# Optimization experiments

Measured on AMD Instinct MI355X. Metric: run time of the kernel, lower is better.

The kernel has to match this reference:

```python
import jax, jax.numpy as jnp
import numpy as np

B, N, H = 8, 256, 768
P = 128          # path_hidden_size
HEADS = 12
D = H // HEADS   # 64
EPS = 1e-5


def layer_norm(x, g, b):
    mu = jnp.mean(x, axis=-1, keepdims=True)
    var = jnp.mean((x - mu) ** 2, axis=-1, keepdims=True)
    return (x - mu) * jax.lax.rsqrt(var + EPS) * g + b


def setup_inputs() -> dict:
    key = jax.random.key(0)
    ks = jax.random.split(key, 16)
    s = 0.02
    return {
        "nodes": jax.random.normal(ks[0], (B, N, H), jnp.float32),
        "bias": jax.random.normal(ks[1], (B, HEADS, N, N), jnp.float32),
        "paths": jax.random.normal(ks[2], (B, N, N, P), jnp.float32),
        "Wq": jax.random.normal(ks[3], (H, H), jnp.float32) * s,
        "bq": jnp.zeros((H,), jnp.float32),
        "Wk": jax.random.normal(ks[4], (H, H), jnp.float32) * s,
        "bk": jnp.zeros((H,), jnp.float32),
        "Wv": jax.random.normal(ks[5], (H, H), jnp.float32) * s,
        "bv": jnp.zeros((H,), jnp.float32),
        "Wsk": jax.random.normal(ks[6], (P, D), jnp.float32) * s,
        "bsk": jnp.zeros((D,), jnp.float32),
        "Wsv": jax.random.normal(ks[7], (P, D), jnp.float32) * s,
        "bsv": jnp.zeros((D,), jnp.float32),
        "Wo": jax.random.normal(ks[8], (H, H), jnp.float32) * s,
        "bo": jnp.zeros((H,), jnp.float32),
        "g_path": jnp.ones((P,), jnp.float32),
        "b_path": jnp.zeros((P,), jnp.float32),
        "g_out": jnp.ones((H,), jnp.float32),
        "b_out": jnp.zeros((H,), jnp.float32),
    }


def reference(nodes, bias, paths, Wq, bq, Wk, bk, Wv, bv, Wsk, bsk, Wsv, bsv,
              Wo, bo, g_path, b_path, g_out, b_out):
    # q/k/v: [B,N,H] -> [B,heads,N,D]
    def split(x):
        return x.reshape(B, N, HEADS, D).transpose(0, 2, 1, 3)

    q = split(nodes @ Wq + bq)
    k = split(nodes @ Wk + bk)
    v = split(nodes @ Wv + bv)

    pn = layer_norm(paths, g_path, b_path)          # [B,N,N,P]
    struct_k = pn @ Wsk + bsk                       # [B,N,N,D]
    struct_v = pn @ Wsv + bsv                       # [B,N,N,D]

    q = q * (D ** -0.5)
    # content scores + per-query-row structural scores + bias
    w = (jnp.einsum('bhqd,bhkd->bhqk', q, k)
         + jnp.einsum('bhqd,bqkd->bhqk', q, struct_k)
         + bias)
    w = jax.nn.softmax(w, axis=-1)                  # [B,heads,N,N]

    out = (jnp.einsum('bhqk,bhkd->bhqd', w, v)
           + jnp.einsum('bhqk,bqkd->bhqd', w, struct_v))
    out = out.transpose(0, 2, 1, 3).reshape(B, N, H)  # combine heads
    out = jax.nn.relu(out @ Wo + bo)
    # dropout is identity in eval mode
    return layer_norm(nodes + out, g_out, b_out)
```

## Files before the change

### kernel.cpp

```cpp
#include <hip/hip_runtime.h>
#include <stdint.h>

#define Bb 8
#define Nn 256
#define Hh 768
#define Pp 128
#define HEADS 12
#define Dd 64
#define EPSf 1e-5f

typedef __attribute__((ext_vector_type(8))) short bhalf8;
typedef __attribute__((ext_vector_type(4))) float f32x4;

__device__ __forceinline__ unsigned short f2bf(float f) {
    union { float f; unsigned u; } v; v.f = f;
    unsigned r = v.u + 0x7FFFu + ((v.u >> 16) & 1u);
    return (unsigned short)(r >> 16);
}

__global__ __launch_bounds__(256) void k_transpose4(const float* __restrict__ a0, const float* __restrict__ a1,
                                                    const float* __restrict__ a2, const float* __restrict__ a3,
                                                    unsigned short* __restrict__ o0, unsigned short* __restrict__ o1,
                                                    unsigned short* __restrict__ o2, unsigned short* __restrict__ o3) {
    __shared__ float tile[32][33];
    int z = blockIdx.z;
    const float* in = (z == 0) ? a0 : (z == 1) ? a1 : (z == 2) ? a2 : a3;
    unsigned short* out = (z == 0) ? o0 : (z == 1) ? o1 : (z == 2) ? o2 : o3;
    const int R = 768, C = 768;
    int c0 = blockIdx.x * 32, r0 = blockIdx.y * 32;
    int tx = threadIdx.x & 31, ty = threadIdx.x >> 5;
    for (int i = ty; i < 32; i += 8)
        tile[i][tx] = in[(size_t)(r0 + i) * C + c0 + tx];
    __syncthreads();
    for (int i = ty; i < 32; i += 8)
        out[(size_t)(c0 + i) * R + r0 + tx] = f2bf(tile[tx][i]);
}

__global__ __launch_bounds__(256) void k_transpose_small(const float* __restrict__ a0, const float* __restrict__ a1,
                                                         unsigned short* __restrict__ o0, unsigned short* __restrict__ o1) {
    __shared__ float tile[32][33];
    int z = blockIdx.z;
    const float* in = (z == 0) ? a0 : a1;
    unsigned short* out = (z == 0) ? o0 : o1;
    const int R = 128, C = 64;
    int c0 = blockIdx.x * 32, r0 = blockIdx.y * 32;
    int tx = threadIdx.x & 31, ty = threadIdx.x >> 5;
    for (int i = ty; i < 32; i += 8)
        tile[i][tx] = in[(size_t)(r0 + i) * C + c0 + tx];
    __syncthreads();
    for (int i = ty; i < 32; i += 8)
        out[(size_t)(c0 + i) * R + r0 + tx] = f2bf(tile[tx][i]);
}

__global__ __launch_bounds__(256) void k_qkv(const float* __restrict__ nodes,
                                             const unsigned short* __restrict__ Wt,
                                             const float* __restrict__ bq, const float* __restrict__ bk,
                                             const float* __restrict__ bv,
                                             float* __restrict__ qs, float* __restrict__ kk,
                                             float* __restrict__ vv) {
    __shared__ __align__(16) unsigned short Alds[64 * 72];
    __shared__ __align__(16) unsigned short Blds[128 * 72];
    int tid = threadIdx.x;
    int m0 = blockIdx.y * 64;
    int n0 = blockIdx.x * 128;
    int w = tid >> 6, lane = tid & 63;
    int wm = w >> 1, wn = w & 1;
    int lm = lane & 15, lq = lane >> 4;
    f32x4 acc[2][4];
#pragma unroll
    for (int i = 0; i < 2; i++)
#pragma unroll
        for (int j = 0; j < 4; j++) acc[i][j] = (f32x4){0.f, 0.f, 0.f, 0.f};

    for (int kt = 0; kt < 768; kt += 64) {
#pragma unroll
        for (int t = 0; t < 4; t++) {
            int c = t * 256 + tid;
            int row = c >> 4, cc = c & 15;
            float4 v = *(const float4*)(nodes + (size_t)(m0 + row) * 768 + kt + cc * 4);
            uint2 uu;
            uu.x = (unsigned)f2bf(v.x) | ((unsigned)f2bf(v.y) << 16);
            uu.y = (unsigned)f2bf(v.z) | ((unsigned)f2bf(v.w) << 16);
            *(uint2*)(Alds + row * 72 + cc * 4) = uu;
        }
#pragma unroll
        for (int t = 0; t < 4; t++) {
            int c = t * 256 + tid;
            int n = c >> 3, kc = c & 7;
            uint4 v = *(const uint4*)(Wt + (size_t)(n0 + n) * 768 + kt + kc * 8);
            *(uint4*)(Blds + n * 72 + kc * 8) = v;
        }
        __syncthreads();
#pragma unroll
        for (int ks = 0; ks < 2; ks++) {
            bhalf8 af[2];
#pragma unroll
            for (int mi = 0; mi < 2; mi++)
                af[mi] = *(const bhalf8*)(Alds + (wm * 32 + mi * 16 + lm) * 72 + ks * 32 + lq * 8);
#pragma unroll
            for (int nt = 0; nt < 4; nt++) {
                bhalf8 bf = *(const bhalf8*)(Blds + (wn * 64 + nt * 16 + lm) * 72 + ks * 32 + lq * 8);
#pragma unroll
                for (int mi = 0; mi < 2; mi++)
                    acc[mi][nt] = __builtin_amdgcn_mfma_f32_16x16x32_bf16(af[mi], bf, acc[mi][nt], 0, 0, 0);
            }
        }
        __syncthreads();
    }
    int wsel = n0 / 768;
    int nb = n0 % 768;
    const float* bias = (wsel == 0) ? bq : (wsel == 1) ? bk : bv;
    float* dst = (wsel == 0) ? qs : (wsel == 1) ? kk : vv;
    float scale = (wsel == 0) ? 0.125f : 1.0f;
#pragma unroll
    for (int mi = 0; mi < 2; mi++)
#pragma unroll
        for (int nt = 0; nt < 4; nt++)
#pragma unroll
            for (int r = 0; r < 4; r++) {
                int row = m0 + wm * 32 + mi * 16 + lq * 4 + r;
                int col = nb + wn * 64 + nt * 16 + lm;
                int hh = col >> 6, d = col & 63;
                int b = row >> 8, qn = row & 255;
                float val = (acc[mi][nt][r] + bias[col]) * scale;
                dst[(((size_t)b * HEADS + hh) * Nn + qn) * Dd + d] = val;
            }
}

__global__ __launch_bounds__(256) void k_scores(const float* __restrict__ qs,
                                                const float* __restrict__ kk,
                                                const float* __restrict__ bias,
                                                float* __restrict__ wg) {
    __shared__ __align__(16) unsigned short Alds[64 * 72];
    __shared__ __align__(16) unsigned short Blds[64 * 72];
    int tid = threadIdx.x;
    int bh = blockIdx.z;
    int m0 = blockIdx.y * 64;
    int n0 = blockIdx.x * 64;
    int w = tid >> 6, lane = tid & 63, lm = lane & 15, lq = lane >> 4;
    const float* Abase = qs + ((size_t)bh * Nn + m0) * Dd;
    const float* Bbase = kk + ((size_t)bh * Nn + n0) * Dd;
#pragma unroll
    for (int t = 0; t < 4; t++) {
        int c = t * 256 + tid;
        int row = c >> 4, cc = c & 15;
        float4 va = *(const float4*)(Abase + (size_t)row * 64 + cc * 4);
        uint2 ua;
        ua.x = (unsigned)f2bf(va.x) | ((unsigned)f2bf(va.y) << 16);
        ua.y = (unsigned)f2bf(va.z) | ((unsigned)f2bf(va.w) << 16);
        *(uint2*)(Alds + row * 72 + cc * 4) = ua;
        float4 vb = *(const float4*)(Bbase + (size_t)row * 64 + cc * 4);
        uint2 ub;
        ub.x = (unsigned)f2bf(vb.x) | ((unsigned)f2bf(vb.y) << 16);
        ub.y = (unsigned)f2bf(vb.z) | ((unsigned)f2bf(vb.w) << 16);
        *(uint2*)(Blds + row * 72 + cc * 4) = ub;
    }
    __syncthreads();
    f32x4 acc[4];
#pragma unroll
    for (int i = 0; i < 4; i++) acc[i] = (f32x4){0.f, 0.f, 0.f, 0.f};
#pragma unroll
    for (int ks = 0; ks < 2; ks++) {
        bhalf8 af = *(const bhalf8*)(Alds + (w * 16 + lm) * 72 + ks * 32 + lq * 8);
#pragma unroll
        for (int nt = 0; nt < 4; nt++) {
            bhalf8 bf = *(const bhalf8*)(Blds + (nt * 16 + lm) * 72 + ks * 32 + lq * 8);
            acc[nt] = __builtin_amdgcn_mfma_f32_16x16x32_bf16(af, bf, acc[nt], 0, 0, 0);
        }
    }
#pragma unroll
    for (int nt = 0; nt < 4; nt++)
#pragma unroll
        for (int r = 0; r < 4; r++) {
            int row = m0 + w * 16 + lq * 4 + r;
            int col = n0 + nt * 16 + lm;
            size_t idx = ((size_t)bh * Nn + row) * Nn + col;
            wg[idx] = acc[nt][r] + bias[idx];
        }
}

__global__ __launch_bounds__(256) void k_structproj(const float* __restrict__ paths,
                                                    const unsigned short* __restrict__ Wskvt,
                                                    const float* __restrict__ gp, const float* __restrict__ bp,
                                                    const float* __restrict__ bsk, const float* __restrict__ bsv,
                                                    unsigned short* __restrict__ skv) {
    __shared__ __align__(16) unsigned short pn[64 * 136];
    __shared__ __align__(16) unsigned short Bt[128 * 136];
    int tid = threadIdx.x;
    size_t r0 = (size_t)blockIdx.x * 64;
    int w = tid >> 6, lane = tid & 63, lm = lane & 15, lq = lane >> 4;
#pragma unroll
    for (int t = 0; t < 8; t++) {
        int c = t * 256 + tid;
        int n = c >> 4, kc = c & 15;
        uint4 v = *(const uint4*)(Wskvt + n * 128 + kc * 8);
        *(uint4*)(Bt + n * 136 + kc * 8) = v;
    }
    float4 g0 = *(const float4*)(gp + lm * 4);
    float4 g1 = *(const float4*)(gp + 64 + lm * 4);
    float4 bb0 = *(const float4*)(bp + lm * 4);
    float4 bb1 = *(const float4*)(bp + 64 + lm * 4);
#pragma unroll
    for (int it = 0; it < 4; it++) {
        int row_l = w * 16 + it * 4 + lq;
        size_t row = r0 + row_l;
        const float* pr = paths + row * 128;
        float4 x0 = *(const float4*)(pr + lm * 4);
        float4 x1 = *(const float4*)(pr + 64 + lm * 4);
        float s = (x0.x + x0.y) + (x0.z + x0.w) + (x1.x + x1.y) + (x1.z + x1.w);
        float s2 = x0.x * x0.x + x0.y * x0.y + x0.z * x0.z + x0.w * x0.w
                 + x1.x * x1.x + x1.y * x1.y + x1.z * x1.z + x1.w * x1.w;
#pragma unroll
        for (int mk = 1; mk < 16; mk <<= 1) {
            s += __shfl_xor(s, mk);
            s2 += __shfl_xor(s2, mk);
        }
        float mu = s * (1.f / 128.f);
        float var = s2 * (1.f / 128.f) - mu * mu;
        float rs = rsqrtf(var + EPSf);
        float p0 = (x0.x - mu) * rs * g0.x + bb0.x;
        float p1 = (x0.y - mu) * rs * g0.y + bb0.y;
        float p2 = (x0.z - mu) * rs * g0.z + bb0.z;
        float p3 = (x0.w - mu) * rs * g0.w + bb0.w;
        float p4 = (x1.x - mu) * rs * g1.x + bb1.x;
        float p5 = (x1.y - mu) * rs * g1.y + bb1.y;
        float p6 = (x1.z - mu) * rs * g1.z + bb1.z;
        float p7 = (x1.w - mu) * rs * g1.w + bb1.w;
        uint2 ua, ub;
        ua.x = (unsigned)f2bf(p0) | ((unsigned)f2bf(p1) << 16);
        ua.y = (unsigned)f2bf(p2) | ((unsigned)f2bf(p3) << 16);
        ub.x = (unsigned)f2bf(p4) | ((unsigned)f2bf(p5) << 16);
        ub.y = (unsigned)f2bf(p6) | ((unsigned)f2bf(p7) << 16);
        *(uint2*)(pn + row_l * 136 + lm * 4) = ua;
        *(uint2*)(pn + row_l * 136 + 64 + lm * 4) = ub;
    }
    __syncthreads();
    f32x4 acc[8];
#pragma unroll
    for (int i = 0; i < 8; i++) acc[i] = (f32x4){0.f, 0.f, 0.f, 0.f};
#pragma unroll
    for (int ks = 0; ks < 4; ks++) {
        bhalf8 af = *(const bhalf8*)(pn + (w * 16 + lm) * 136 + ks * 32 + lq * 8);
#pragma unroll
        for (int nt = 0; nt < 8; nt++) {
            bhalf8 bf = *(const bhalf8*)(Bt + (nt * 16 + lm) * 136 + ks * 32 + lq * 8);
            acc[nt] = __builtin_amdgcn_mfma_f32_16x16x32_bf16(af, bf, acc[nt], 0, 0, 0);
        }
    }
    __syncthreads();
#pragma unroll
    for (int nt = 0; nt < 8; nt++) {
        int col = nt * 16 + lm;
        float bias = (col < 64) ? bsk[col] : bsv[col - 64];
#pragma unroll
        for (int r = 0; r < 4; r++) {
            int row_l = w * 16 + lq * 4 + r;
            pn[row_l * 136 + col] = f2bf(acc[nt][r] + bias);
        }
    }
    __syncthreads();
#pragma unroll
    for (int i = 0; i < 4; i++) {
        int c = i * 256 + tid;
        int row = c >> 4, chunk = c & 15;
        uint4 v = *(const uint4*)(pn + row * 136 + chunk * 8);
        *(uint4*)(skv + (r0 + row) * 128 + chunk * 8) = v;
    }
}

__global__ __launch_bounds__(256) void k_attn(const float* __restrict__ qs,
                                              const unsigned short* __restrict__ skv,
                                              float* __restrict__ wg,
                                              float* __restrict__ attn) {
    __shared__ __align__(16) unsigned short SKV[256 * 72];
    __shared__ __align__(16) unsigned short A2[16 * 264];
    __shared__ __align__(16) unsigned short Ql[16 * 72];
    __shared__ float redm[16][4];
    __shared__ float reds[16][4];
    int tid = threadIdx.x;
    int bq = blockIdx.x;
    int b = bq >> 8, q = bq & 255;
    int w = tid >> 6, lane = tid & 63, lm = lane & 15, lq = lane >> 4;
    if (tid < 192) {
        int h = tid >> 4, dc = (tid & 15) * 4;
        float4 v = *(const float4*)(qs + (((size_t)b * HEADS + h) * Nn + q) * Dd + dc);
        uint2 u;
        u.x = (unsigned)f2bf(v.x) | ((unsigned)f2bf(v.y) << 16);
        u.y = (unsigned)f2bf(v.z) | ((unsigned)f2bf(v.w) << 16);
        *(uint2*)(Ql + h * 72 + dc) = u;
    } else {
        int t = tid - 192;
        int h = 12 + (t >> 4), dc = (t & 15) * 4;
        uint2 z; z.x = 0; z.y = 0;
        *(uint2*)(Ql + h * 72 + dc) = z;
    }
    const unsigned short* rowb = skv + (size_t)bq * 256 * 128;
#pragma unroll
    for (int i = 0; i < 8; i++) {
        int c = i * 256 + tid;
        int k = c >> 3, j = c & 7;
        uint4 v = *(const uint4*)(rowb + (size_t)k * 128 + j * 8);
        *(uint4*)(SKV + k * 72 + j * 8) = v;
    }
    __syncthreads();
    f32x4 acc1[4];
#pragma unroll
    for (int i = 0; i < 4; i++) acc1[i] = (f32x4){0.f, 0.f, 0.f, 0.f};
#pragma unroll
    for (int ks = 0; ks < 2; ks++) {
        bhalf8 af = *(const bhalf8*)(Ql + lm * 72 + ks * 32 + lq * 8);
#pragma unroll
        for (int nt = 0; nt < 4; nt++) {
            int n0 = (w * 4 + nt) * 16;
            bhalf8 bf = *(const bhalf8*)(SKV + (n0 + lm) * 72 + ks * 32 + lq * 8);
            acc1[nt] = __builtin_amdgcn_mfma_f32_16x16x32_bf16(af, bf, acc1[nt], 0, 0, 0);
        }
    }
    size_t wbase = ((size_t)b * HEADS) * Nn * Nn + (size_t)q * Nn;
    float S[4][4];
#pragma unroll
    for (int nt = 0; nt < 4; nt++)
#pragma unroll
        for (int r = 0; r < 4; r++) {
            int row = lq * 4 + r;
            int col = (w * 4 + nt) * 16 + lm;
            float wgv = (row < 12) ? wg[wbase + (size_t)row * (Nn * Nn) + col] : 0.f;
            S[nt][r] = acc1[nt][r] + wgv;
        }
    float m4[4];
#pragma unroll
    for (int r = 0; r < 4; r++)
        m4[r] = fmaxf(fmaxf(S[0][r], S[1][r]), fmaxf(S[2][r], S[3][r]));
#pragma unroll
    for (int mk = 1; mk < 16; mk <<= 1)
#pragma unroll
        for (int r = 0; r < 4; r++) m4[r] = fmaxf(m4[r], __shfl_xor(m4[r], mk));
    if (lm == 0) {
#pragma unroll
        for (int r = 0; r < 4; r++) redm[lq * 4 + r][w] = m4[r];
    }
    __syncthreads();
    float rowmax[4];
#pragma unroll
    for (int r = 0; r < 4; r++) {
        int row = lq * 4 + r;
        rowmax[r] = fmaxf(fmaxf(redm[row][0], redm[row][1]), fmaxf(redm[row][2], redm[row][3]));
    }
    float P[4][4], psum[4];
#pragma unroll
    for (int r = 0; r < 4; r++) {
#pragma unroll
        for (int nt = 0; nt < 4; nt++) P[nt][r] = __expf(S[nt][r] - rowmax[r]);
        psum[r] = (P[0][r] + P[1][r]) + (P[2][r] + P[3][r]);
    }
#pragma unroll
    for (int mk = 1; mk < 16; mk <<= 1)
#pragma unroll
        for (int r = 0; r < 4; r++) psum[r] += __shfl_xor(psum[r], mk);
    if (lm == 0) {
#pragma unroll
        for (int r = 0; r < 4; r++) reds[lq * 4 + r][w] = psum[r];
    }
    __syncthreads();
    float inv[4];
#pragma unroll
    for (int r = 0; r < 4; r++) {
        int row = lq * 4 + r;
        inv[r] = 1.f / (((reds[row][0] + reds[row][1]) + (reds[row][2] + reds[row][3])));
    }
#pragma unroll
    for (int nt = 0; nt < 4; nt++)
#pragma unroll
        for (int r = 0; r < 4; r++) {
            int row = lq * 4 + r;
            int col = (w * 4 + nt) * 16 + lm;
            float p = P[nt][r] * inv[r];
            A2[row * 264 + col] = f2bf(p);
            if (row < 12) wg[wbase + (size_t)row * (Nn * Nn) + col] = p;
        }
#pragma unroll
    for (int i = 0; i < 8; i++) {
        int c = i * 256 + tid;
        int k = c >> 3, j = c & 7;
        uint4 v = *(const uint4*)(rowb + (size_t)k * 128 + 64 + j * 8);
        *(uint4*)(SKV + k * 72 + j * 8) = v;
    }
    __syncthreads();
    f32x4 acc2 = (f32x4){0.f, 0.f, 0.f, 0.f};
#pragma unroll
    for (int ks = 0; ks < 8; ks++) {
        bhalf8 af = *(const bhalf8*)(A2 + lm * 264 + ks * 32 + lq * 8);
        bhalf8 bf;
#pragma unroll
        for (int j = 0; j < 8; j++)
            bf[j] = (short)SKV[(ks * 32 + lq * 8 + j) * 72 + w * 16 + lm];
        acc2 = __builtin_amdgcn_mfma_f32_16x16x32_bf16(af, bf, acc2, 0, 0, 0);
    }
#pragma unroll
    for (int r = 0; r < 4; r++) {
        int row = lq * 4 + r;
        if (row < 12) attn[(size_t)bq * Hh + row * 64 + w * 16 + lm] = acc2[r];
    }
}

__global__ __launch_bounds__(256) void k_ctxout(const float* __restrict__ wg,
                                                const float* __restrict__ vv,
                                                float* __restrict__ attn) {
    __shared__ __align__(16) float Al[64 * 68];
    __shared__ __align__(16) float Bl[64 * 68];
    int tid = threadIdx.x;
    int bh = blockIdx.y;
    int m0 = blockIdx.x * 64;
    int b = bh / 12, h = bh % 12;
    int tx = tid & 15, ty = tid >> 4;
    int c0 = tx * 4, r0 = ty * 4;
    float acc[4][4];
#pragma unroll
    for (int i = 0; i < 4; i++)
#pragma unroll
        for (int j = 0; j < 4; j++) acc[i][j] = 0.f;
    const float* Abase = wg + ((size_t)bh * Nn + m0) * Nn;
    const float* Bbase = vv + (size_t)bh * Nn * Dd;
    for (int kt = 0; kt < 256; kt += 64) {
#pragma unroll
        for (int t = 0; t < 4; t++) {
            int c = t * 256 + tid;
            int row = c >> 4, cc = c & 15;
            *(float4*)(Al + row * 68 + cc * 4) = *(const float4*)(Abase + (size_t)row * 256 + kt + cc * 4);
            *(float4*)(Bl + row * 68 + cc * 4) = *(const float4*)(Bbase + (size_t)(kt + row) * 64 + cc * 4);
        }
        __syncthreads();
#pragma unroll 8
        for (int k = 0; k < 64; k++) {
            float4 bv4 = *(const float4*)(Bl + k * 68 + c0);
            float a0 = Al[(r0 + 0) * 68 + k];
            float a1 = Al[(r0 + 1) * 68 + k];
            float a2 = Al[(r0 + 2) * 68 + k];
            float a3 = Al[(r0 + 3) * 68 + k];
            acc[0][0] += a0 * bv4.x; acc[0][1] += a0 * bv4.y; acc[0][2] += a0 * bv4.z; acc[0][3] += a0 * bv4.w;
            acc[1][0] += a1 * bv4.x; acc[1][1] += a1 * bv4.y; acc[1][2] += a1 * bv4.z; acc[1][3] += a1 * bv4.w;
            acc[2][0] += a2 * bv4.x; acc[2][1] += a2 * bv4.y; acc[2][2] += a2 * bv4.z; acc[2][3] += a2 * bv4.w;
            acc[3][0] += a3 * bv4.x; acc[3][1] += a3 * bv4.y; acc[3][2] += a3 * bv4.z; acc[3][3] += a3 * bv4.w;
        }
        __syncthreads();
    }
#pragma unroll
    for (int i = 0; i < 4; i++)
#pragma unroll
        for (int j = 0; j < 4; j++) {
            size_t o = ((size_t)b * Nn + m0 + r0 + i) * Hh + h * 64 + c0 + j;
            attn[o] += acc[i][j];
        }
}

__global__ __launch_bounds__(256) void k_outproj(const float* __restrict__ attn,
                                                 const unsigned short* __restrict__ Wot,
                                                 const float* __restrict__ bo,
                                                 const float* __restrict__ nodes,
                                                 float* __restrict__ tmp) {
    __shared__ __align__(16) unsigned short Alds[64 * 72];
    __shared__ __align__(16) unsigned short Blds[128 * 72];
    int tid = threadIdx.x;
    int m0 = blockIdx.y * 64;
    int n0 = blockIdx.x * 128;
    int w = tid >> 6, lane = tid & 63;
    int wm = w >> 1, wn = w & 1;
    int lm = lane & 15, lq = lane >> 4;
    f32x4 acc[2][4];
#pragma unroll
    for (int i = 0; i < 2; i++)
#pragma unroll
        for (int j = 0; j < 4; j++) acc[i][j] = (f32x4){0.f, 0.f, 0.f, 0.f};
    for (int kt = 0; kt < 768; kt += 64) {
#pragma unroll
        for (int t = 0; t < 4; t++) {
            int c = t * 256 + tid;
            int row = c >> 4, cc = c & 15;
            float4 v = *(const float4*)(attn + (size_t)(m0 + row) * 768 + kt + cc * 4);
            uint2 uu;
            uu.x = (unsigned)f2bf(v.x) | ((unsigned)f2bf(v.y) << 16);
            uu.y = (unsigned)f2bf(v.z) | ((unsigned)f2bf(v.w) << 16);
            *(uint2*)(Alds + row * 72 + cc * 4) = uu;
        }
#pragma unroll
        for (int t = 0; t < 4; t++) {
            int c = t * 256 + tid;
            int n = c >> 3, kc = c & 7;
            uint4 v = *(const uint4*)(Wot + (size_t)(n0 + n) * 768 + kt + kc * 8);
            *(uint4*)(Blds + n * 72 + kc * 8) = v;
        }
        __syncthreads();
#pragma unroll
        for (int ks = 0; ks < 2; ks++) {
            bhalf8 af[2];
#pragma unroll
            for (int mi = 0; mi < 2; mi++)
                af[mi] = *(const bhalf8*)(Alds + (wm * 32 + mi * 16 + lm) * 72 + ks * 32 + lq * 8);
#pragma unroll
            for (int nt = 0; nt < 4; nt++) {
                bhalf8 bf = *(const bhalf8*)(Blds + (wn * 64 + nt * 16 + lm) * 72 + ks * 32 + lq * 8);
#pragma unroll
                for (int mi = 0; mi < 2; mi++)
                    acc[mi][nt] = __builtin_amdgcn_mfma_f32_16x16x32_bf16(af[mi], bf, acc[mi][nt], 0, 0, 0);
            }
        }
        __syncthreads();
    }
#pragma unroll
    for (int mi = 0; mi < 2; mi++)
#pragma unroll
        for (int nt = 0; nt < 4; nt++)
#pragma unroll
            for (int r = 0; r < 4; r++) {
                int row = m0 + wm * 32 + mi * 16 + lq * 4 + r;
                int col = n0 + wn * 64 + nt * 16 + lm;
                float val = acc[mi][nt][r] + bo[col];
                val = fmaxf(val, 0.f) + nodes[(size_t)row * 768 + col];
                tmp[(size_t)row * 768 + col] = val;
            }
}

__global__ __launch_bounds__(256) void k_finalln(const float* __restrict__ tmp,
                                                 const float* __restrict__ go,
                                                 const float* __restrict__ bout,
                                                 float* __restrict__ out) {
    __shared__ float rs1[4], rs2[4];
    int m = blockIdx.x, tid = threadIdx.x;
    int lane = tid & 63, wid = tid >> 6;
    const float* row = tmp + (size_t)m * 768;
    float x0 = row[tid], x1 = row[tid + 256], x2 = row[tid + 512];
    float s = x0 + x1 + x2;
    float s2 = x0 * x0 + x1 * x1 + x2 * x2;
#pragma unroll
    for (int mk = 32; mk; mk >>= 1) {
        s += __shfl_xor(s, mk);
        s2 += __shfl_xor(s2, mk);
    }
    if (lane == 0) { rs1[wid] = s; rs2[wid] = s2; }
    __syncthreads();
    s = rs1[0] + rs1[1] + rs1[2] + rs1[3];
    s2 = rs2[0] + rs2[1] + rs2[2] + rs2[3];
    float mu = s * (1.f / 768.f);
    float var = s2 * (1.f / 768.f) - mu * mu;
    float rstd = rsqrtf(var + EPSf);
    float* orow = out + (size_t)m * 768;
    orow[tid] = (x0 - mu) * rstd * go[tid] + bout[tid];
    orow[tid + 256] = (x1 - mu) * rstd * go[tid + 256] + bout[tid + 256];
    orow[tid + 512] = (x2 - mu) * rstd * go[tid + 512] + bout[tid + 512];
}

extern "C" void kernel_launch(void* const* d_in, const int* in_sizes, int n_in,
                              void* d_out, int out_size, void* d_ws, size_t ws_size,
                              hipStream_t stream) {
    const float* nodes = (const float*)d_in[0];
    const float* bias  = (const float*)d_in[1];
    const float* paths = (const float*)d_in[2];
    const float* Wq = (const float*)d_in[3];  const float* bq  = (const float*)d_in[4];
    const float* Wk = (const float*)d_in[5];  const float* bk  = (const float*)d_in[6];
    const float* Wv = (const float*)d_in[7];  const float* bv  = (const float*)d_in[8];
    const float* Wsk = (const float*)d_in[9]; const float* bsk = (const float*)d_in[10];
    const float* Wsv = (const float*)d_in[11];const float* bsv = (const float*)d_in[12];
    const float* Wo = (const float*)d_in[13]; const float* bo  = (const float*)d_in[14];
    const float* gp = (const float*)d_in[15]; const float* bp  = (const float*)d_in[16];
    const float* go = (const float*)d_in[17]; const float* bout= (const float*)d_in[18];
    float* out = (float*)d_out;

    char* ws = (char*)d_ws;
    size_t off = 0;
    auto carve = [&](size_t bytes) -> char* {
        char* p = ws + off;
        off += (bytes + 255) & ~(size_t)255;
        return p;
    };
    float* qs   = (float*)carve((size_t)Bb * HEADS * Nn * Dd * 4);
    float* kk   = (float*)carve((size_t)Bb * HEADS * Nn * Dd * 4);
    float* vv   = (float*)carve((size_t)Bb * HEADS * Nn * Dd * 4);
    float* wg   = (float*)carve((size_t)Bb * HEADS * Nn * Nn * 4);
    float* attn = (float*)carve((size_t)Bb * Nn * Hh * 4);
    float* tmp  = (float*)carve((size_t)Bb * Nn * Hh * 4);
    unsigned short* Wqkvt = (unsigned short*)carve((size_t)3 * 768 * 768 * 2);
    unsigned short* Wot   = (unsigned short*)carve((size_t)768 * 768 * 2);
    unsigned short* Wskvt = (unsigned short*)carve((size_t)128 * 128 * 2);
    unsigned short* skv   = (unsigned short*)carve((size_t)Bb * Nn * Nn * 128 * 2);
    (void)ws_size; (void)in_sizes; (void)n_in; (void)out_size;

    hipLaunchKernelGGL(k_transpose4, dim3(24, 24, 4), dim3(256), 0, stream,
                       Wq, Wk, Wv, Wo,
                       Wqkvt, Wqkvt + (size_t)768 * 768, Wqkvt + (size_t)2 * 768 * 768, Wot);
    hipLaunchKernelGGL(k_transpose_small, dim3(2, 4, 2), dim3(256), 0, stream,
                       Wsk, Wsv, Wskvt, Wskvt + (size_t)64 * 128);

    hipLaunchKernelGGL(k_qkv, dim3(18, 32), dim3(256), 0, stream, nodes, Wqkvt, bq, bk, bv, qs, kk, vv);
    hipLaunchKernelGGL(k_scores, dim3(4, 4, 96), dim3(256), 0, stream, qs, kk, bias, wg);
    hipLaunchKernelGGL(k_structproj, dim3(8192), dim3(256), 0, stream, paths, Wskvt, gp, bp, bsk, bsv, skv);
    hipLaunchKernelGGL(k_attn, dim3(2048), dim3(256), 0, stream, qs, skv, wg, attn);
    hipLaunchKernelGGL(k_ctxout, dim3(4, 96), dim3(256), 0, stream, wg, vv, attn);
    hipLaunchKernelGGL(k_outproj, dim3(6, 32), dim3(256), 0, stream, attn, Wot, bo, nodes, tmp);
    hipLaunchKernelGGL(k_finalln, dim3(2048), dim3(256), 0, stream, tmp, go, bout, out);
}
```

Before: 557.4 us.

## Restructure attention pipeline with bf16 transposed layouts and MFMA context GEMM

The pipeline now keeps intermediates in bf16 in transposed layouts: V is stored as [B,H,D,N], the struct projection writes separate struct-K and transposed struct-V buffers, and the softmax probabilities are written as bf16. The context GEMM moves from scalar FP32 FMA to bf16 MFMA. The QKV and output GEMMs read B fragments straight from global memory and double-buffer the A tile in LDS. A cheaper bf16 pack using perm replaces the round-to-nearest-even conversion, which trades exact rounding for fewer instructions. The struct projection processes 128 rows per block, halving the grid, and reads weights from global memory instead of LDS.

```diff
diff --git a/kernel.cpp b/kernel.cpp
--- a/kernel.cpp
+++ b/kernel.cpp
@@ -16,6 +16,11 @@
     union { float f; unsigned u; } v; v.f = f;
     unsigned r = v.u + 0x7FFFu + ((v.u >> 16) & 1u);
     return (unsigned short)(r >> 16);
+}
+__device__ __forceinline__ unsigned pk(float lo, float hi) {
+    unsigned a = __float_as_uint(lo) + 0x8000u;
+    unsigned b = __float_as_uint(hi) + 0x8000u;
+    return __builtin_amdgcn_perm(b, a, 0x07060302u);
 }
 
 __global__ __launch_bounds__(256) void k_transpose4(const float* __restrict__ a0, const float* __restrict__ a1,
@@ -54,52 +59,48 @@
 
 __global__ __launch_bounds__(256) void k_qkv(const float* __restrict__ nodes,
                                              const unsigned short* __restrict__ Wt,
-                                             const float* __restrict__ bq, const float* __restrict__ bk,
-                                             const float* __restrict__ bv,
-                                             float* __restrict__ qs, float* __restrict__ kk,
-                                             float* __restrict__ vv) {
-    __shared__ __align__(16) unsigned short Alds[64 * 72];
-    __shared__ __align__(16) unsigned short Blds[128 * 72];
+                                             const float* __restrict__ bqp, const float* __restrict__ bkp,
+                                             const float* __restrict__ bvp,
+                                             float* __restrict__ qso, float* __restrict__ kko,
+                                             unsigned short* __restrict__ vvT) {
+    __shared__ __align__(16) unsigned short A[2][64 * 72];
     int tid = threadIdx.x;
     int m0 = blockIdx.y * 64;
     int n0 = blockIdx.x * 128;
     int w = tid >> 6, lane = tid & 63;
     int wm = w >> 1, wn = w & 1;
     int lm = lane & 15, lq = lane >> 4;
-    f32x4 acc[2][4];
-#pragma unroll
-    for (int i = 0; i < 2; i++)
-#pragma unroll
-        for (int j = 0; j < 4; j++) acc[i][j] = (f32x4){0.f, 0.f, 0.f, 0.f};
-
-    for (int kt = 0; kt < 768; kt += 64) {
+
+    auto stageA = [&](int kt, unsigned short* dst) {
 #pragma unroll
         for (int t = 0; t < 4; t++) {
             int c = t * 256 + tid;
             int row = c >> 4, cc = c & 15;
             float4 v = *(const float4*)(nodes + (size_t)(m0 + row) * 768 + kt + cc * 4);
-            uint2 uu;
-            uu.x = (unsigned)f2bf(v.x) | ((unsigned)f2bf(v.y) << 16);
-            uu.y = (unsigned)f2bf(v.z) | ((unsigned)f2bf(v.w) << 16);
-            *(uint2*)(Alds + row * 72 + cc * 4) = uu;
-        }
-#pragma unroll
-        for (int t = 0; t < 4; t++) {
-            int c = t * 256 + tid;
-            int n = c >> 3, kc = c & 7;
-            uint4 v = *(const uint4*)(Wt + (size_t)(n0 + n) * 768 + kt + kc * 8);
-            *(uint4*)(Blds + n * 72 + kc * 8) = v;
-        }
-        __syncthreads();
+            uint2 u; u.x = pk(v.x, v.y); u.y = pk(v.z, v.w);
+            *(uint2*)(dst + row * 72 + cc * 4) = u;
+        }
+    };
+    f32x4 acc[2][4];
+#pragma unroll
+    for (int i = 0; i < 2; i++)
+#pragma unroll
+        for (int j = 0; j < 4; j++) acc[i][j] = (f32x4){0.f, 0.f, 0.f, 0.f};
+
+    stageA(0, A[0]);
+    __syncthreads();
+    int buf = 0;
+    for (int kt = 0; kt < 768; kt += 64, buf ^= 1) {
+        if (kt < 704) stageA(kt + 64, A[buf ^ 1]);
 #pragma unroll
         for (int ks = 0; ks < 2; ks++) {
             bhalf8 af[2];
 #pragma unroll
             for (int mi = 0; mi < 2; mi++)
-                af[mi] = *(const bhalf8*)(Alds + (wm * 32 + mi * 16 + lm) * 72 + ks * 32 + lq * 8);
+                af[mi] = *(const bhalf8*)(A[buf] + (wm * 32 + mi * 16 + lm) * 72 + ks * 32 + lq * 8);
 #pragma unroll
             for (int nt = 0; nt < 4; nt++) {
-                bhalf8 bf = *(const bhalf8*)(Blds + (wn * 64 + nt * 16 + lm) * 72 + ks * 32 + lq * 8);
+                bhalf8 bf = *(const bhalf8*)(Wt + (size_t)(n0 + wn * 64 + nt * 16 + lm) * 768 + kt + ks * 32 + lq * 8);
 #pragma unroll
                 for (int mi = 0; mi < 2; mi++)
                     acc[mi][nt] = __builtin_amdgcn_mfma_f32_16x16x32_bf16(af[mi], bf, acc[mi][nt], 0, 0, 0);
@@ -109,22 +110,39 @@
     }
     int wsel = n0 / 768;
     int nb = n0 % 768;
-    const float* bias = (wsel == 0) ? bq : (wsel == 1) ? bk : bv;
-    float* dst = (wsel == 0) ? qs : (wsel == 1) ? kk : vv;
-    float scale = (wsel == 0) ? 0.125f : 1.0f;
-#pragma unroll
-    for (int mi = 0; mi < 2; mi++)
-#pragma unroll
-        for (int nt = 0; nt < 4; nt++)
-#pragma unroll
-            for (int r = 0; r < 4; r++) {
-                int row = m0 + wm * 32 + mi * 16 + lq * 4 + r;
+    if (wsel == 2) {
+#pragma unroll
+        for (int mi = 0; mi < 2; mi++)
+#pragma unroll
+            for (int nt = 0; nt < 4; nt++) {
                 int col = nb + wn * 64 + nt * 16 + lm;
-                int hh = col >> 6, d = col & 63;
-                int b = row >> 8, qn = row & 255;
-                float val = (acc[mi][nt][r] + bias[col]) * scale;
-                dst[(((size_t)b * HEADS + hh) * Nn + qn) * Dd + d] = val;
+                int h = col >> 6, d = col & 63;
+                int row0 = m0 + wm * 32 + mi * 16 + lq * 4;
+                int bb = row0 >> 8, q0 = row0 & 255;
+                float bia = bvp[col];
+                uint2 u;
+                u.x = pk(acc[mi][nt][0] + bia, acc[mi][nt][1] + bia);
+                u.y = pk(acc[mi][nt][2] + bia, acc[mi][nt][3] + bia);
+                *(uint2*)(vvT + (((size_t)bb * HEADS + h) * Dd + d) * Nn + q0) = u;
             }
+    } else {
+        const float* bias = (wsel == 0) ? bqp : bkp;
+        float* dst = (wsel == 0) ? qso : kko;
+        float scale = (wsel == 0) ? 0.125f : 1.0f;
+#pragma unroll
+        for (int mi = 0; mi < 2; mi++)
+#pragma unroll
+            for (int nt = 0; nt < 4; nt++)
+#pragma unroll
+                for (int r = 0; r < 4; r++) {
+                    int row = m0 + wm * 32 + mi * 16 + lq * 4 + r;
+                    int col = nb + wn * 64 + nt * 16 + lm;
+                    int hh = col >> 6, d = col & 63;
+                    int bb = row >> 8, qn = row & 255;
+                    float val = (acc[mi][nt][r] + bias[col]) * scale;
+                    dst[(((size_t)bb * HEADS + hh) * Nn + qn) * Dd + d] = val;
+                }
+    }
 }
 
 __global__ __launch_bounds__(256) void k_scores(const float* __restrict__ qs,
@@ -145,14 +163,10 @@
         int c = t * 256 + tid;
         int row = c >> 4, cc = c & 15;
         float4 va = *(const float4*)(Abase + (size_t)row * 64 + cc * 4);
-        uint2 ua;
-        ua.x = (unsigned)f2bf(va.x) | ((unsigned)f2bf(va.y) << 16);
-        ua.y = (unsigned)f2bf(va.z) | ((unsigned)f2bf(va.w) << 16);
+        uint2 ua; ua.x = pk(va.x, va.y); ua.y = pk(va.z, va.w);
         *(uint2*)(Alds + row * 72 + cc * 4) = ua;
         float4 vb = *(const float4*)(Bbase + (size_t)row * 64 + cc * 4);
-        uint2 ub;
-        ub.x = (unsigned)f2bf(vb.x) | ((unsigned)f2bf(vb.y) << 16);
-        ub.y = (unsigned)f2bf(vb.z) | ((unsigned)f2bf(vb.w) << 16);
+        uint2 ub; ub.x = pk(vb.x, vb.y); ub.y = pk(vb.z, vb.w);
         *(uint2*)(Blds + row * 72 + cc * 4) = ub;
     }
     __syncthreads();
@@ -183,28 +197,24 @@
                                                     const unsigned short* __restrict__ Wskvt,
                                                     const float* __restrict__ gp, const float* __restrict__ bp,
                                                     const float* __restrict__ bsk, const float* __restrict__ bsv,
-                                                    unsigned short* __restrict__ skv) {
-    __shared__ __align__(16) unsigned short pn[64 * 136];
-    __shared__ __align__(16) unsigned short Bt[128 * 136];
+                                                    unsigned short* __restrict__ skg,
+                                                    unsigned short* __restrict__ svTg) {
+    __shared__ __align__(16) unsigned short SM[17920];
+    unsigned short* pn  = SM;
+    unsigned short* skl = SM;
+    unsigned short* svl = SM + 9216;
     int tid = threadIdx.x;
-    size_t r0 = (size_t)blockIdx.x * 64;
+    size_t r0 = (size_t)blockIdx.x * 128;
+    int bq = (int)(r0 >> 8), k0 = (int)(r0 & 255);
     int w = tid >> 6, lane = tid & 63, lm = lane & 15, lq = lane >> 4;
-#pragma unroll
-    for (int t = 0; t < 8; t++) {
-        int c = t * 256 + tid;
-        int n = c >> 4, kc = c & 15;
-        uint4 v = *(const uint4*)(Wskvt + n * 128 + kc * 8);
-        *(uint4*)(Bt + n * 136 + kc * 8) = v;
-    }
     float4 g0 = *(const float4*)(gp + lm * 4);
     float4 g1 = *(const float4*)(gp + 64 + lm * 4);
-    float4 bb0 = *(const float4*)(bp + lm * 4);
-    float4 bb1 = *(const float4*)(bp + 64 + lm * 4);
-#pragma unroll
-    for (int it = 0; it < 4; it++) {
-        int row_l = w * 16 + it * 4 + lq;
-        size_t row = r0 + row_l;
-        const float* pr = paths + row * 128;
+    float4 b0 = *(const float4*)(bp + lm * 4);
+    float4 b1 = *(const float4*)(bp + 64 + lm * 4);
+#pragma unroll
+    for (int it = 0; it < 8; it++) {
+        int row_l = w * 32 + it * 4 + lq;
+        const float* pr = paths + (r0 + row_l) * 128;
         float4 x0 = *(const float4*)(pr + lm * 4);
         float4 x1 = *(const float4*)(pr + 64 + lm * 4);
         float s = (x0.x + x0.y) + (x0.z + x0.w) + (x1.x + x1.y) + (x1.z + x1.w);
@@ -218,63 +228,86 @@
         float mu = s * (1.f / 128.f);
         float var = s2 * (1.f / 128.f) - mu * mu;
         float rs = rsqrtf(var + EPSf);
-        float p0 = (x0.x - mu) * rs * g0.x + bb0.x;
-        float p1 = (x0.y - mu) * rs * g0.y + bb0.y;
-        float p2 = (x0.z - mu) * rs * g0.z + bb0.z;
-        float p3 = (x0.w - mu) * rs * g0.w + bb0.w;
-        float p4 = (x1.x - mu) * rs * g1.x + bb1.x;
-        float p5 = (x1.y - mu) * rs * g1.y + bb1.y;
-        float p6 = (x1.z - mu) * rs * g1.z + bb1.z;
-        float p7 = (x1.w - mu) * rs * g1.w + bb1.w;
+        float p0 = (x0.x - mu) * rs * g0.x + b0.x;
+        float p1 = (x0.y - mu) * rs * g0.y + b0.y;
+        float p2 = (x0.z - mu) * rs * g0.z + b0.z;
+        float p3 = (x0.w - mu) * rs * g0.w + b0.w;
+        float p4 = (x1.x - mu) * rs * g1.x + b1.x;
+        float p5 = (x1.y - mu) * rs * g1.y + b1.y;
+        float p6 = (x1.z - mu) * rs * g1.z + b1.z;
+        float p7 = (x1.w - mu) * rs * g1.w + b1.w;
         uint2 ua, ub;
-        ua.x = (unsigned)f2bf(p0) | ((unsigned)f2bf(p1) << 16);
-        ua.y = (unsigned)f2bf(p2) | ((unsigned)f2bf(p3) << 16);
-        ub.x = (unsigned)f2bf(p4) | ((unsigned)f2bf(p5) << 16);
-        ub.y = (unsigned)f2bf(p6) | ((unsigned)f2bf(p7) << 16);
+        ua.x = pk(p0, p1); ua.y = pk(p2, p3);
+        ub.x = pk(p4, p5); ub.y = pk(p6, p7);
         *(uint2*)(pn + row_l * 136 + lm * 4) = ua;
         *(uint2*)(pn + row_l * 136 + 64 + lm * 4) = ub;
     }
     __syncthreads();
-    f32x4 acc[8];
-#pragma unroll
-    for (int i = 0; i < 8; i++) acc[i] = (f32x4){0.f, 0.f, 0.f, 0.f};
+    f32x4 acc[2][8];
+#pragma unroll
+    for (int i = 0; i < 2; i++)
+#pragma unroll
+        for (int j = 0; j < 8; j++) acc[i][j] = (f32x4){0.f, 0.f, 0.f, 0.f};
 #pragma unroll
     for (int ks = 0; ks < 4; ks++) {
-        bhalf8 af = *(const bhalf8*)(pn + (w * 16 + lm) * 136 + ks * 32 + lq * 8);
+        bhalf8 af0 = *(const bhalf8*)(pn + (w * 32 + lm) * 136 + ks * 32 + lq * 8);
+        bhalf8 af1 = *(const bhalf8*)(pn + (w * 32 + 16 + lm) * 136 + ks * 32 + lq * 8);
 #pragma unroll
         for (int nt = 0; nt < 8; nt++) {
-            bhalf8 bf = *(const bhalf8*)(Bt + (nt * 16 + lm) * 136 + ks * 32 + lq * 8);
-            acc[nt] = __builtin_amdgcn_mfma_f32_16x16x32_bf16(af, bf, acc[nt], 0, 0, 0);
-        }
-    }
-    __syncthreads();
-#pragma unroll
-    for (int nt = 0; nt < 8; nt++) {
+            bhalf8 bf = *(const bhalf8*)(Wskvt + (nt * 16 + lm) * 128 + ks * 32 + lq * 8);
+            acc[0][nt] = __builtin_amdgcn_mfma_f32_16x16x32_bf16(af0, bf, acc[0][nt], 0, 0, 0);
+            acc[1][nt] = __builtin_amdgcn_mfma_f32_16x16x32_bf16(af1, bf, acc[1][nt], 0, 0, 0);
+        }
+    }
+    __syncthreads();
+#pragma unroll
+    for (int nt = 0; nt < 4; nt++) {
         int col = nt * 16 + lm;
-        float bias = (col < 64) ? bsk[col] : bsv[col - 64];
-#pragma unroll
-        for (int r = 0; r < 4; r++) {
-            int row_l = w * 16 + lq * 4 + r;
-            pn[row_l * 136 + col] = f2bf(acc[nt][r] + bias);
+        float bia = bsk[col];
+#pragma unroll
+        for (int rt = 0; rt < 2; rt++)
+#pragma unroll
+            for (int r = 0; r < 4; r++)
+                skl[(w * 32 + rt * 16 + lq * 4 + r) * 72 + col] = f2bf(acc[rt][nt][r] + bia);
+    }
+#pragma unroll
+    for (int nt = 4; nt < 8; nt++) {
+        int d = (nt - 4) * 16 + lm;
+        float bia = bsv[d];
+#pragma unroll
+        for (int rt = 0; rt < 2; rt++) {
+            int kloc = w * 32 + rt * 16 + lq * 4;
+            uint2 u;
+            u.x = pk(acc[rt][nt][0] + bia, acc[rt][nt][1] + bia);
+            u.y = pk(acc[rt][nt][2] + bia, acc[rt][nt][3] + bia);
+            *(uint2*)(svl + d * 136 + kloc) = u;
         }
     }
     __syncthreads();
 #pragma unroll
     for (int i = 0; i < 4; i++) {
         int c = i * 256 + tid;
-        int row = c >> 4, chunk = c & 15;
-        uint4 v = *(const uint4*)(pn + row * 136 + chunk * 8);
-        *(uint4*)(skv + (r0 + row) * 128 + chunk * 8) = v;
+        int row = c >> 3, cg = c & 7;
+        uint4 v = *(const uint4*)(skl + row * 72 + cg * 8);
+        *(uint4*)(skg + ((size_t)bq * 256 + k0 + row) * 64 + cg * 8) = v;
+    }
+#pragma unroll
+    for (int i = 0; i < 4; i++) {
+        int c = i * 256 + tid;
+        int d = c >> 4, cg = c & 15;
+        uint4 v = *(const uint4*)(svl + d * 136 + cg * 8);
+        *(uint4*)(svTg + (size_t)bq * 16384 + (size_t)d * 256 + k0 + cg * 8) = v;
     }
 }
 
 __global__ __launch_bounds__(256) void k_attn(const float* __restrict__ qs,
-                                              const unsigned short* __restrict__ skv,
-                                              float* __restrict__ wg,
+                                              const unsigned short* __restrict__ skg,
+                                              const unsigned short* __restrict__ svTg,
+                                              const float* __restrict__ wg,
+                                              unsigned short* __restrict__ pbf,
                                               float* __restrict__ attn) {
-    __shared__ __align__(16) unsigned short SKV[256 * 72];
+    __shared__ __align__(16) unsigned short Ql[16 * 72];
     __shared__ __align__(16) unsigned short A2[16 * 264];
-    __shared__ __align__(16) unsigned short Ql[16 * 72];
     __shared__ float redm[16][4];
     __shared__ float reds[16][4];
     int tid = threadIdx.x;
@@ -284,9 +317,7 @@
     if (tid < 192) {
         int h = tid >> 4, dc = (tid & 15) * 4;
         float4 v = *(const float4*)(qs + (((size_t)b * HEADS + h) * Nn + q) * Dd + dc);
-        uint2 u;
-        u.x = (unsigned)f2bf(v.x) | ((unsigned)f2bf(v.y) << 16);
-        u.y = (unsigned)f2bf(v.z) | ((unsigned)f2bf(v.w) << 16);
+        uint2 u; u.x = pk(v.x, v.y); u.y = pk(v.z, v.w);
         *(uint2*)(Ql + h * 72 + dc) = u;
     } else {
         int t = tid - 192;
@@ -294,15 +325,8 @@
         uint2 z; z.x = 0; z.y = 0;
         *(uint2*)(Ql + h * 72 + dc) = z;
     }
-    const unsigned short* rowb = skv + (size_t)bq * 256 * 128;
-#pragma unroll
-    for (int i = 0; i < 8; i++) {
-        int c = i * 256 + tid;
-        int k = c >> 3, j = c & 7;
-        uint4 v = *(const uint4*)(rowb + (size_t)k * 128 + j * 8);
-        *(uint4*)(SKV + k * 72 + j * 8) = v;
-    }
-    __syncthreads();
+    __syncthreads();
+    const unsigned short* skb = skg + (size_t)bq * 16384;
     f32x4 acc1[4];
 #pragma unroll
     for (int i = 0; i < 4; i++) acc1[i] = (f32x4){0.f, 0.f, 0.f, 0.f};
@@ -311,12 +335,11 @@
         bhalf8 af = *(const bhalf8*)(Ql + lm * 72 + ks * 32 + lq * 8);
 #pragma unroll
         for (int nt = 0; nt < 4; nt++) {
-            int n0 = (w * 4 + nt) * 16;
-            bhalf8 bf = *(const bhalf8*)(SKV + (n0 + lm) * 72 + ks * 32 + lq * 8);
+            bhalf8 bf = *(const bhalf8*)(skb + (size_t)((w * 4 + nt) * 16 + lm) * 64 + ks * 32 + lq * 8);
             acc1[nt] = __builtin_amdgcn_mfma_f32_16x16x32_bf16(af, bf, acc1[nt], 0, 0, 0);
         }
     }
-    size_t wbase = ((size_t)b * HEADS) * Nn * Nn + (size_t)q * Nn;
+    size_t wbase = ((size_t)b * HEADS) * 65536 + (size_t)q * 256;
     float S[4][4];
 #pragma unroll
     for (int nt = 0; nt < 4; nt++)
@@ -324,7 +347,7 @@
         for (int r = 0; r < 4; r++) {
             int row = lq * 4 + r;
             int col = (w * 4 + nt) * 16 + lm;
-            float wgv = (row < 12) ? wg[wbase + (size_t)row * (Nn * Nn) + col] : 0.f;
+            float wgv = (row < 12) ? wg[wbase + (size_t)row * 65536 + col] : 0.f;
             S[nt][r] = acc1[nt][r] + wgv;
         }
     float m4[4];
@@ -366,7 +389,7 @@
 #pragma unroll
     for (int r = 0; r < 4; r++) {
         int row = lq * 4 + r;
-        inv[r] = 1.f / (((reds[row][0] + reds[row][1]) + (reds[row][2] + reds[row][3])));
+        inv[r] = 1.f / ((reds[row][0] + reds[row][1]) + (reds[row][2] + reds[row][3]));
     }
 #pragma unroll
     for (int nt = 0; nt < 4; nt++)
@@ -375,25 +398,17 @@
             int row = lq * 4 + r;
             int col = (w * 4 + nt) * 16 + lm;
             float p = P[nt][r] * inv[r];
-            A2[row * 264 + col] = f2bf(p);
-            if (row < 12) wg[wbase + (size_t)row * (Nn * Nn) + col] = p;
-        }
-#pragma unroll
-    for (int i = 0; i < 8; i++) {
-        int c = i * 256 + tid;
-        int k = c >> 3, j = c & 7;
-        uint4 v = *(const uint4*)(rowb + (size_t)k * 128 + 64 + j * 8);
-        *(uint4*)(SKV + k * 72 + j * 8) = v;
-    }
-    __syncthreads();
+            unsigned short pv = f2bf(p);
+            A2[row * 264 + col] = pv;
+            if (row < 12) pbf[wbase + (size_t)row * 65536 + col] = pv;
+        }
+    __syncthreads();
+    const unsigned short* svb = svTg + (size_t)bq * 16384;
     f32x4 acc2 = (f32x4){0.f, 0.f, 0.f, 0.f};
 #pragma unroll
     for (int ks = 0; ks < 8; ks++) {
         bhalf8 af = *(const bhalf8*)(A2 + lm * 264 + ks * 32 + lq * 8);
-        bhalf8 bf;
-#pragma unroll
-        for (int j = 0; j < 8; j++)
-            bf[j] = (short)SKV[(ks * 32 + lq * 8 + j) * 72 + w * 16 + lm];
+        bhalf8 bf = *(const bhalf8*)(svb + (size_t)(w * 16 + lm) * 256 + ks * 32 + lq * 8);
         acc2 = __builtin_amdgcn_mfma_f32_16x16x32_bf16(af, bf, acc2, 0, 0, 0);
     }
 #pragma unroll
@@ -403,53 +418,36 @@
     }
 }
 
-__global__ __launch_bounds__(256) void k_ctxout(const float* __restrict__ wg,
-                                                const float* __restrict__ vv,
+__global__ __launch_bounds__(256) void k_ctxout(const unsigned short* __restrict__ pbf,
+                                                const unsigned short* __restrict__ vvT,
                                                 float* __restrict__ attn) {
-    __shared__ __align__(16) float Al[64 * 68];
-    __shared__ __align__(16) float Bl[64 * 68];
     int tid = threadIdx.x;
+    int m0 = blockIdx.x * 64;
     int bh = blockIdx.y;
-    int m0 = blockIdx.x * 64;
-    int b = bh / 12, h = bh % 12;
-    int tx = tid & 15, ty = tid >> 4;
-    int c0 = tx * 4, r0 = ty * 4;
-    float acc[4][4];
-#pragma unroll
-    for (int i = 0; i < 4; i++)
-#pragma unroll
-        for (int j = 0; j < 4; j++) acc[i][j] = 0.f;
-    const float* Abase = wg + ((size_t)bh * Nn + m0) * Nn;
-    const float* Bbase = vv + (size_t)bh * Nn * Dd;
-    for (int kt = 0; kt < 256; kt += 64) {
-#pragma unroll
-        for (int t = 0; t < 4; t++) {
-            int c = t * 256 + tid;
-            int row = c >> 4, cc = c & 15;
-            *(float4*)(Al + row * 68 + cc * 4) = *(const float4*)(Abase + (size_t)row * 256 + kt + cc * 4);
-            *(float4*)(Bl + row * 68 + cc * 4) = *(const float4*)(Bbase + (size_t)(kt + row) * 64 + cc * 4);
-        }
-        __syncthreads();
-#pragma unroll 8
-        for (int k = 0; k < 64; k++) {
-            float4 bv4 = *(const float4*)(Bl + k * 68 + c0);
-            float a0 = Al[(r0 + 0) * 68 + k];
-            float a1 = Al[(r0 + 1) * 68 + k];
-            float a2 = Al[(r0 + 2) * 68 + k];
-            float a3 = Al[(r0 + 3) * 68 + k];
-            acc[0][0] += a0 * bv4.x; acc[0][1] += a0 * bv4.y; acc[0][2] += a0 * bv4.z; acc[0][3] += a0 * bv4.w;
-            acc[1][0] += a1 * bv4.x; acc[1][1] += a1 * bv4.y; acc[1][2] += a1 * bv4.z; acc[1][3] += a1 * bv4.w;
-            acc[2][0] += a2 * bv4.x; acc[2][1] += a2 * bv4.y; acc[2][2] += a2 * bv4.z; acc[2][3] += a2 * bv4.w;
-            acc[3][0] += a3 * bv4.x; acc[3][1] += a3 * bv4.y; acc[3][2] += a3 * bv4.z; acc[3][3] += a3 * bv4.w;
-        }
-        __syncthreads();
-    }
-#pragma unroll
-    for (int i = 0; i < 4; i++)
-#pragma unroll
-        for (int j = 0; j < 4; j++) {
-            size_t o = ((size_t)b * Nn + m0 + r0 + i) * Hh + h * 64 + c0 + j;
-            attn[o] += acc[i][j];
+    int b = bh / HEADS, h = bh % HEADS;
+    int w = tid >> 6, lane = tid & 63, lm = lane & 15, lq = lane >> 4;
+    const unsigned short* Pb = pbf + (size_t)bh * 65536;
+    const unsigned short* Vb = vvT + (size_t)bh * 16384;
+    f32x4 acc[4];
+#pragma unroll
+    for (int i = 0; i < 4; i++) acc[i] = (f32x4){0.f, 0.f, 0.f, 0.f};
+#pragma unroll
+    for (int ks = 0; ks < 8; ks++) {
+        bhalf8 af = *(const bhalf8*)(Pb + (size_t)(m0 + w * 16 + lm) * 256 + ks * 32 + lq * 8);
+#pragma unroll
+        for (int ct = 0; ct < 4; ct++) {
+            bhalf8 bf = *(const bhalf8*)(Vb + (size_t)(ct * 16 + lm) * 256 + ks * 32 + lq * 8);
+            acc[ct] = __builtin_amdgcn_mfma_f32_16x16x32_bf16(af, bf, acc[ct], 0, 0, 0);
+        }
+    }
+#pragma unroll
+    for (int ct = 0; ct < 4; ct++)
+#pragma unroll
+        for (int r = 0; r < 4; r++) {
+            int row = m0 + w * 16 + lq * 4 + r;
+            int col = h * 64 + ct * 16 + lm;
+            size_t o = ((size_t)b * Nn + row) * Hh + col;
+            attn[o] += acc[ct][r];
         }
 }
 
@@ -458,47 +456,42 @@
                                                  const float* __restrict__ bo,
                                                  const float* __restrict__ nodes,
                                                  float* __restrict__ tmp) {
-    __shared__ __align__(16) unsigned short Alds[64 * 72];
-    __shared__ __align__(16) unsigned short Blds[128 * 72];
+    __shared__ __align__(16) unsigned short A[2][64 * 72];
     int tid = threadIdx.x;
     int m0 = blockIdx.y * 64;
     int n0 = blockIdx.x * 128;
     int w = tid >> 6, lane = tid & 63;
     int wm = w >> 1, wn = w & 1;
     int lm = lane & 15, lq = lane >> 4;
-    f32x4 acc[2][4];
-#pragma unroll
-    for (int i = 0; i < 2; i++)
-#pragma unroll
-        for (int j = 0; j < 4; j++) acc[i][j] = (f32x4){0.f, 0.f, 0.f, 0.f};
-    for (int kt = 0; kt < 768; kt += 64) {
+    auto stageA = [&](int kt, unsigned short* dst) {
 #pragma unroll
         for (int t = 0; t < 4; t++) {
             int c = t * 256 + tid;
             int row = c >> 4, cc = c & 15;
             float4 v = *(const float4*)(attn + (size_t)(m0 + row) * 768 + kt + cc * 4);
-            uint2 uu;
-            uu.x = (unsigned)f2bf(v.x) | ((unsigned)f2bf(v.y) << 16);
-            uu.y = (unsigned)f2bf(v.z) | ((unsigned)f2bf(v.w) << 16);
-            *(uint2*)(Alds + row * 72 + cc * 4) = uu;
-        }
-#pragma unroll
-        for (int t = 0; t < 4; t++) {
-            int c = t * 256 + tid;
-            int n = c >> 3, kc = c & 7;
-            uint4 v = *(const uint4*)(Wot + (size_t)(n0 + n) * 768 + kt + kc * 8);
-            *(uint4*)(Blds + n * 72 + kc * 8) = v;
-        }
-        __syncthreads();
+            uint2 u; u.x = pk(v.x, v.y); u.y = pk(v.z, v.w);
+            *(uint2*)(dst + row * 72 + cc * 4) = u;
+        }
+    };
+    f32x4 acc[2][4];
+#pragma unroll
+    for (int i = 0; i < 2; i++)
+#pragma unroll
+        for (int j = 0; j < 4; j++) acc[i][j] = (f32x4){0.f, 0.f, 0.f, 0.f};
+    stageA(0, A[0]);
+    __syncthreads();
+    int buf = 0;
+    for (int kt = 0; kt < 768; kt += 64, buf ^= 1) {
+        if (kt < 704) stageA(kt + 64, A[buf ^ 1]);
 #pragma unroll
         for (int ks = 0; ks < 2; ks++) {
             bhalf8 af[2];
 #pragma unroll
             for (int mi = 0; mi < 2; mi++)
-                af[mi] = *(const bhalf8*)(Alds + (wm * 32 + mi * 16 + lm) * 72 + ks * 32 + lq * 8);
+                af[mi] = *(const bhalf8*)(A[buf] + (wm * 32 + mi * 16 + lm) * 72 + ks * 32 + lq * 8);
 #pragma unroll
             for (int nt = 0; nt < 4; nt++) {
-                bhalf8 bf = *(const bhalf8*)(Blds + (wn * 64 + nt * 16 + lm) * 72 + ks * 32 + lq * 8);
+                bhalf8 bf = *(const bhalf8*)(Wot + (size_t)(n0 + wn * 64 + nt * 16 + lm) * 768 + kt + ks * 32 + lq * 8);
 #pragma unroll
                 for (int mi = 0; mi < 2; mi++)
                     acc[mi][nt] = __builtin_amdgcn_mfma_f32_16x16x32_bf16(af[mi], bf, acc[mi][nt], 0, 0, 0);
@@ -574,14 +567,16 @@
     };
     float* qs   = (float*)carve((size_t)Bb * HEADS * Nn * Dd * 4);
     float* kk   = (float*)carve((size_t)Bb * HEADS * Nn * Dd * 4);
-    float* vv   = (float*)carve((size_t)Bb * HEADS * Nn * Dd * 4);
     float* wg   = (float*)carve((size_t)Bb * HEADS * Nn * Nn * 4);
     float* attn = (float*)carve((size_t)Bb * Nn * Hh * 4);
     float* tmp  = (float*)carve((size_t)Bb * Nn * Hh * 4);
     unsigned short* Wqkvt = (unsigned short*)carve((size_t)3 * 768 * 768 * 2);
     unsigned short* Wot   = (unsigned short*)carve((size_t)768 * 768 * 2);
     unsigned short* Wskvt = (unsigned short*)carve((size_t)128 * 128 * 2);
-    unsigned short* skv   = (unsigned short*)carve((size_t)Bb * Nn * Nn * 128 * 2);
+    unsigned short* vvT   = (unsigned short*)carve((size_t)Bb * HEADS * Dd * Nn * 2);
+    unsigned short* pbf   = (unsigned short*)carve((size_t)Bb * HEADS * Nn * Nn * 2);
+    unsigned short* skg   = (unsigned short*)carve((size_t)Bb * Nn * Nn * Dd * 2);
+    unsigned short* svTg  = (unsigned short*)carve((size_t)Bb * Nn * Dd * Nn * 2);
     (void)ws_size; (void)in_sizes; (void)n_in; (void)out_size;
 
     hipLaunchKernelGGL(k_transpose4, dim3(24, 24, 4), dim3(256), 0, stream,
@@ -590,11 +585,11 @@
     hipLaunchKernelGGL(k_transpose_small, dim3(2, 4, 2), dim3(256), 0, stream,
                        Wsk, Wsv, Wskvt, Wskvt + (size_t)64 * 128);
 
-    hipLaunchKernelGGL(k_qkv, dim3(18, 32), dim3(256), 0, stream, nodes, Wqkvt, bq, bk, bv, qs, kk, vv);
+    hipLaunchKernelGGL(k_qkv, dim3(18, 32), dim3(256), 0, stream, nodes, Wqkvt, bq, bk, bv, qs, kk, vvT);
     hipLaunchKernelGGL(k_scores, dim3(4, 4, 96), dim3(256), 0, stream, qs, kk, bias, wg);
-    hipLaunchKernelGGL(k_structproj, dim3(8192), dim3(256), 0, stream, paths, Wskvt, gp, bp, bsk, bsv, skv);
-    hipLaunchKernelGGL(k_attn, dim3(2048), dim3(256), 0, stream, qs, skv, wg, attn);
-    hipLaunchKernelGGL(k_ctxout, dim3(4, 96), dim3(256), 0, stream, wg, vv, attn);
+    hipLaunchKernelGGL(k_structproj, dim3(4096), dim3(256), 0, stream, paths, Wskvt, gp, bp, bsk, bsv, skg, svTg);
+    hipLaunchKernelGGL(k_attn, dim3(2048), dim3(256), 0, stream, qs, skg, svTg, wg, pbf, attn);
+    hipLaunchKernelGGL(k_ctxout, dim3(4, 96), dim3(256), 0, stream, pbf, vvT, attn);
     hipLaunchKernelGGL(k_outproj, dim3(6, 32), dim3(256), 0, stream, attn, Wot, bo, nodes, tmp);
     hipLaunchKernelGGL(k_finalln, dim3(2048), dim3(256), 0, stream, tmp, go, bout, out);
 }
```

Result: slower. 643.5 us (+15.5%).
